# Optimization experiments

Measured on AMD Instinct MI355X. Metric: run time of the kernel, lower is better.

The kernel has to match this reference:

```python
import jax, jax.numpy as jnp
import numpy as np
from jax import lax

LRELU_SLOPE = 0.01  # torch nn.LeakyReLU default
BN_EPS = 1e-5


def _conv3(x, w, b):
    # LatticePad(3x3 stencil, center (1,1)) + LatticeConvolution on 'cp' lattice == SAME 3x3 conv
    y = lax.conv_general_dilated(x, w, (1, 1), 'SAME', dimension_numbers=('NCHW', 'OIHW', 'NCHW'))
    return y + b[None, :, None, None]


def _lrelu(x):
    return jnp.where(x >= 0, x, LRELU_SLOPE * x)


def _down2(x):
    # LatticeDownsample with D=[[2,0],[0,2]] on cp lattice: keep even coords
    return x[:, :, ::2, ::2]


def _up2(x):
    # LatticeUpsample with D=[[2,0],[0,2]]: zero insertion
    n, c, h, w = x.shape
    return jnp.zeros((n, c, 2 * h, 2 * w), x.dtype).at[:, :, ::2, ::2].set(x)


def setup_inputs() -> dict:
    key = jax.random.key(0)
    ks = iter(jax.random.split(key, 32))

    def w3(ci, co):
        return jax.random.normal(next(ks), (co, ci, 3, 3), jnp.float32) * (1.0 / np.sqrt(ci * 9.0))

    chans = [3, 64, 128, 256, 512, 1024]
    inp = {"x": jax.random.normal(next(ks), (2, 3, 512, 512), jnp.float32)}
    for i in range(5):
        inp[f"w_d{i}"] = w3(chans[i], chans[i + 1])
        inp[f"b_d{i}"] = jnp.zeros((chans[i + 1],), jnp.float32)
    inp["w_in"] = w3(1024, 1024)
    inp["b_in"] = jnp.zeros((1024,), jnp.float32)
    inp["gamma"] = jnp.ones((1024,), jnp.float32)
    inp["beta"] = jnp.zeros((1024,), jnp.float32)
    up_io = [(1024, 512), (512, 256), (256, 128), (128, 64), (64, 64)]
    for i, (ci, co) in enumerate(up_io):
        inp[f"w_u{i}"] = w3(ci, co)
        inp[f"b_u{i}"] = jnp.zeros((co,), jnp.float32)
    inp["w_ep"] = jax.random.normal(next(ks), (3, 64), jnp.float32) * 0.125
    inp["b_ep"] = jnp.zeros((3,), jnp.float32)
    return inp


def reference(x, w_d0, b_d0, w_d1, b_d1, w_d2, b_d2, w_d3, b_d3, w_d4, b_d4,
              w_in, b_in, gamma, beta,
              w_u0, b_u0, w_u1, b_u1, w_u2, b_u2, w_u3, b_u3, w_u4, b_u4,
              w_ep, b_ep):
    h = x
    # encoder: conv3x3 + LeakyReLU, then stride-2 subsample (skip outputs unused: skip=False in config)
    for w, b in [(w_d0, b_d0), (w_d1, b_d1), (w_d2, b_d2), (w_d3, b_d3), (w_d4, b_d4)]:
        h = _down2(_lrelu(_conv3(h, w, b)))
    # innermost ConvBlock: conv + BatchNorm (batch stats, training mode) + LeakyReLU
    h = _conv3(h, w_in, b_in)
    mu = h.mean((0, 2, 3), keepdims=True)
    var = h.var((0, 2, 3), keepdims=True)
    h = (h - mu) / jnp.sqrt(var + BN_EPS) * gamma[None, :, None, None] + beta[None, :, None, None]
    h = _lrelu(h)
    # decoder: zero-insert upsample, conv3x3 + LeakyReLU
    for w, b in [(w_u0, b_u0), (w_u1, b_u1), (w_u2, b_u2), (w_u3, b_u3), (w_u4, b_u4)]:
        h = _lrelu(_conv3(_up2(h), w, b))
    # epilogue 1x1 conv
    return jnp.einsum('nchw,oc->nohw', h, w_ep) + b_ep[None, :, None, None]
```

## Files before the change

kernel.cpp:

```cpp
#include <hip/hip_runtime.h>
#include <math.h>

#define LRELU_SLOPE 0.01f
#define BN_EPS 1e-5f

__device__ __forceinline__ float lrelu_f(float v) { return v >= 0.f ? v : LRELU_SLOPE * v; }

template <int MODE, int CC, bool PARTIAL>
__global__ __launch_bounds__(256, 2) void conv3_kernel(
    const float* __restrict__ in, const float* __restrict__ wgt,
    const float* __restrict__ bias, float* __restrict__ out,
    int Cin, int Hin, int Win, int Cout, int Ho, int Wo, int apply_act,
    int segCi, int cogY, size_t seg_stride)
{
  constexpr int IH = (MODE == 1) ? 17 : 10;
  constexpr int IW = (MODE == 1) ? 33 : 18;
  constexpr int IP = (MODE == 1) ? 36 : 20;
  __shared__ __align__(16) float s_in[CC * IH * IP];
  __shared__ __align__(16) float s_w[CC * 9 * 64];

  const int tid = threadIdx.x;
  const int tx  = tid & 15;
  const int ty  = tid >> 4;
  const int row = ty >> 1;
  const int xh  = (ty & 1) * 8;

  const int tilesX = Wo >> 4;
  const int x0   = (blockIdx.x % tilesX) * 16;
  const int y0   = (blockIdx.x / tilesX) * 8;
  const int cog0 = (blockIdx.y % cogY) * 64;
  const int seg  = blockIdx.y / cogY;
  const int ci_begin = seg * segCi;
  const int n    = blockIdx.z;
  if (PARTIAL) out += (size_t)seg * seg_stride;

  const size_t HWin = (size_t)Hin * Win;
  const float* inN = in + (size_t)n * Cin * HWin;

  float acc[4][8];
#pragma unroll
  for (int a = 0; a < 4; a++)
#pragma unroll
    for (int b = 0; b < 8; b++) acc[a][b] = 0.f;

  for (int ci0 = 0; ci0 < segCi; ci0 += CC) {
    const int chunk = (segCi - ci0 < CC) ? (segCi - ci0) : CC;
    __syncthreads();
    const int tot = chunk * (IH * IW);
    for (int idx = tid; idx < tot; idx += 256) {
      const int ci  = idx / (IH * IW);
      const int rem = idx - ci * (IH * IW);
      const int r   = rem / IW;
      const int c   = rem - r * IW;
      float v = 0.f;
      const int gci = ci_begin + ci0 + ci;
      if (MODE == 1) {
        const int gy = 2 * y0 - 1 + r;
        const int gx = 2 * x0 - 1 + c;
        if (gy >= 0 && gy < Hin && gx >= 0 && gx < Win)
          v = inN[(size_t)gci * HWin + (size_t)gy * Win + gx];
        const int dst = (c & 1) ? (20 + (c >> 1)) : (c >> 1);
        s_in[(ci * IH + r) * IP + dst] = v;
      } else {
        const int gy = y0 - 1 + r;
        const int gx = x0 - 1 + c;
        if (gy >= 0 && gy < Hin && gx >= 0 && gx < Win)
          v = inN[(size_t)gci * HWin + (size_t)gy * Win + gx];
        s_in[(ci * IH + r) * IP + c] = v;
      }
    }
    const int e9 = chunk * 9;
    const int wtot = e9 * 64;
    for (int idx = tid; idx < wtot; idx += 256) {
      const int co = idx & 63;
      const int e  = idx >> 6;
      s_w[e * 64 + co] = wgt[(size_t)(cog0 + co) * Cin * 9 + (size_t)(ci_begin + ci0) * 9 + e];
    }
    __syncthreads();

    auto body = [&](int ci) {
#pragma unroll
      for (int ky = 0; ky < 3; ky++) {
        if (MODE == 1) {
          const int base = (ci * IH + 2 * row + ky) * IP;
          const float4 ea = *(const float4*)&s_in[base + xh];
          const float4 eb = *(const float4*)&s_in[base + xh + 4];
          const float  e8 = s_in[base + xh + 8];
          const float4 oa = *(const float4*)&s_in[base + 20 + xh];
          const float4 ob = *(const float4*)&s_in[base + 24 + xh];
          const float ev[9] = {ea.x, ea.y, ea.z, ea.w, eb.x, eb.y, eb.z, eb.w, e8};
          const float ov[8] = {oa.x, oa.y, oa.z, oa.w, ob.x, ob.y, ob.z, ob.w};
#pragma unroll
          for (int kx = 0; kx < 3; kx++) {
            const int e = ci * 9 + ky * 3 + kx;
            const float4 w4 = *(const float4*)&s_w[e * 64 + (tx << 2)];
            const float wv[4] = {w4.x, w4.y, w4.z, w4.w};
#pragma unroll
            for (int j = 0; j < 8; j++) {
              const float xv = (kx == 0) ? ev[j] : ((kx == 1) ? ov[j] : ev[j + 1]);
#pragma unroll
              for (int k = 0; k < 4; k++) acc[k][j] += wv[k] * xv;
            }
          }
        } else {
          const int base = (ci * IH + row + ky) * IP + xh;
          const float4 a4 = *(const float4*)&s_in[base];
          const float4 b4 = *(const float4*)&s_in[base + 4];
          const float2 c2 = *(const float2*)&s_in[base + 8];
          const float iv[10] = {a4.x, a4.y, a4.z, a4.w, b4.x, b4.y, b4.z, b4.w, c2.x, c2.y};
#pragma unroll
          for (int kx = 0; kx < 3; kx++) {
            const int e = ci * 9 + ky * 3 + kx;
            const float4 w4 = *(const float4*)&s_w[e * 64 + (tx << 2)];
            const float wv[4] = {w4.x, w4.y, w4.z, w4.w};
#pragma unroll
            for (int j = 0; j < 8; j++) {
              const float xv = iv[j + kx];
#pragma unroll
              for (int k = 0; k < 4; k++) acc[k][j] += wv[k] * xv;
            }
          }
        }
      }
    };
    if (chunk == CC) {
#pragma unroll
      for (int ci = 0; ci < CC; ci++) body(ci);
    } else {
      for (int ci = 0; ci < chunk; ci++) body(ci);
    }
  }

#pragma unroll
  for (int k = 0; k < 4; k++) {
    const int co = cog0 + tx * 4 + k;
    float* op = out + ((size_t)((size_t)n * Cout + co) * Ho + (y0 + row)) * Wo + x0 + xh;
    float4 v0, v1;
    if constexpr (PARTIAL) {
      v0.x = acc[k][0]; v0.y = acc[k][1]; v0.z = acc[k][2]; v0.w = acc[k][3];
      v1.x = acc[k][4]; v1.y = acc[k][5]; v1.z = acc[k][6]; v1.w = acc[k][7];
    } else {
      const float b = bias[co];
      v0.x = acc[k][0] + b; v0.y = acc[k][1] + b; v0.z = acc[k][2] + b; v0.w = acc[k][3] + b;
      v1.x = acc[k][4] + b; v1.y = acc[k][5] + b; v1.z = acc[k][6] + b; v1.w = acc[k][7] + b;
      if (apply_act) {
        v0.x = lrelu_f(v0.x); v0.y = lrelu_f(v0.y); v0.z = lrelu_f(v0.z); v0.w = lrelu_f(v0.w);
        v1.x = lrelu_f(v1.x); v1.y = lrelu_f(v1.y); v1.z = lrelu_f(v1.z); v1.w = lrelu_f(v1.w);
      }
    }
    *reinterpret_cast<float4*>(op) = v0;
    *reinterpret_cast<float4*>(op + 4) = v1;
  }
}

template <int NQ, int KCO, int CC, bool EPI, bool PARTIAL>
__global__ __launch_bounds__(256, 2) void up_conv_kernel(
    const float* __restrict__ in, const float* __restrict__ wgt,
    const float* __restrict__ bias, float* __restrict__ out,
    int Cin, int Hin, int Win, int Cout, int Ho, int Wo,
    int segCi, int cogY, size_t seg_stride,
    const float* __restrict__ w_ep, const float* __restrict__ b_ep)
{
  constexpr int NCO = 16 * KCO;
  constexpr int LOG = (KCO == 4) ? 6 : 5;
  constexpr int TQ = 2 * NQ;
  constexpr int T  = 4 * TQ;
  constexpr int IR = 4 * NQ + 1;
  constexpr int PR = IR + 1;
  __shared__ __align__(16) float s_in[CC * IR * PR];
  __shared__ __align__(16) float s_w[CC * 9 * NCO];
  __shared__ float s_epi[EPI ? 3 * 16 * 17 : 1];

  const int tid = threadIdx.x;
  const int tx  = tid & 15;
  const int ty  = tid >> 4;
  const int Qy  = ty >> 2;
  const int Qx  = ty & 3;

  const int tilesX = Wo / T;
  const int x0   = (blockIdx.x % tilesX) * T;
  const int y0   = (blockIdx.x / tilesX) * T;
  const int cog0 = (blockIdx.y % cogY) * NCO;
  const int seg  = blockIdx.y / cogY;
  const int ci_begin = seg * segCi;
  const int n    = blockIdx.z;
  if (PARTIAL) out += (size_t)seg * seg_stride;
  const int r0 = y0 >> 1;
  const int c0 = x0 >> 1;

  const size_t HWin = (size_t)Hin * Win;
  const float* inN = in + (size_t)n * Cin * HWin;

  float acc[KCO][TQ][TQ];
#pragma unroll
  for (int k = 0; k < KCO; k++)
#pragma unroll
    for (int i = 0; i < TQ; i++)
#pragma unroll
      for (int j = 0; j < TQ; j++) acc[k][i][j] = 0.f;

  for (int ci0 = 0; ci0 < segCi; ci0 += CC) {
    __syncthreads();
    const int tot = CC * (IR * IR);
    for (int idx = tid; idx < tot; idx += 256) {
      const int ci  = idx / (IR * IR);
      const int rem = idx - ci * (IR * IR);
      const int r   = rem / IR;
      const int c   = rem - r * IR;
      const int gy = r0 + r, gx = c0 + c;
      float v = 0.f;
      if (gy < Hin && gx < Win)
        v = inN[(size_t)(ci_begin + ci0 + ci) * HWin + (size_t)gy * Win + gx];
      s_in[(ci * IR + r) * PR + c] = v;
    }
    const int wtot = CC * 9 * NCO;
    for (int idx = tid; idx < wtot; idx += 256) {
      const int co = idx & (NCO - 1);
      const int e  = idx >> LOG;
      s_w[e * NCO + co] = wgt[(size_t)(cog0 + co) * Cin * 9 + (size_t)(ci_begin + ci0) * 9 + e];
    }
    __syncthreads();

#pragma unroll
    for (int ci = 0; ci < CC; ci++) {
      float iv[NQ + 1][NQ + 1];
#pragma unroll
      for (int dr = 0; dr <= NQ; dr++)
#pragma unroll
        for (int dc = 0; dc <= NQ; dc++)
          iv[dr][dc] = s_in[(ci * IR + NQ * Qy + dr) * PR + NQ * Qx + dc];
#pragma unroll
      for (int t = 0; t < 9; t++) {
        const int ky = t / 3, kx = t % 3;
        float wv[KCO];
        if constexpr (KCO == 4) {
          const float4 w4 = *(const float4*)&s_w[(ci * 9 + t) * 64 + (tx << 2)];
          wv[0] = w4.x; wv[1] = w4.y; wv[2] = w4.z; wv[3] = w4.w;
        } else {
          const float2 w2 = *(const float2*)&s_w[(ci * 9 + t) * 32 + (tx << 1)];
          wv[0] = w2.x; wv[1] = w2.y;
        }
        const int pr  = (ky == 1) ? 0 : 1;
        const int drr = (ky == 2) ? 1 : 0;
        const int pc  = (kx == 1) ? 0 : 1;
        const int dcc = (kx == 2) ? 1 : 0;
#pragma unroll
        for (int a = 0; a < NQ; a++)
#pragma unroll
          for (int b = 0; b < NQ; b++) {
            const float xv = iv[a + drr][b + dcc];
#pragma unroll
            for (int k = 0; k < KCO; k++)
              acc[k][2 * a + pr][2 * b + pc] += wv[k] * xv;
          }
      }
    }
  }

  if (!EPI) {
#pragma unroll
    for (int k = 0; k < KCO; k++) {
      const int co = cog0 + tx * KCO + k;
      const float bv = PARTIAL ? 0.f : bias[co];
#pragma unroll
      for (int i = 0; i < TQ; i++) {
        const int y = y0 + TQ * Qy + i;
        float* op = out + ((size_t)((size_t)n * Cout + co) * Ho + y) * Wo + x0 + TQ * Qx;
        if constexpr (NQ == 2) {
          float4 v;
          if constexpr (PARTIAL) {
            v.x = acc[k][i][0]; v.y = acc[k][i][1]; v.z = acc[k][i][2]; v.w = acc[k][i][3];
          } else {
            v.x = lrelu_f(acc[k][i][0] + bv); v.y = lrelu_f(acc[k][i][1] + bv);
            v.z = lrelu_f(acc[k][i][2] + bv); v.w = lrelu_f(acc[k][i][3] + bv);
          }
          *reinterpret_cast<float4*>(op) = v;
        } else {
          float2 v;
          if constexpr (PARTIAL) {
            v.x = acc[k][i][0]; v.y = acc[k][i][1];
          } else {
            v.x = lrelu_f(acc[k][i][0] + bv); v.y = lrelu_f(acc[k][i][1] + bv);
          }
          *reinterpret_cast<float2*>(op) = v;
        }
      }
    }
  } else {
    float wep[3][KCO];
#pragma unroll
    for (int o = 0; o < 3; o++)
#pragma unroll
      for (int k = 0; k < KCO; k++) wep[o][k] = w_ep[o * 64 + tx * KCO + k];
    const float bv[KCO] = {bias[tx * KCO + 0], bias[tx * KCO + 1],
                           bias[tx * KCO + 2], bias[tx * KCO + 3]};
    __syncthreads();
#pragma unroll
    for (int i = 0; i < TQ; i++)
#pragma unroll
      for (int j = 0; j < TQ; j++) {
        float h[KCO];
#pragma unroll
        for (int k = 0; k < KCO; k++) h[k] = lrelu_f(acc[k][i][j] + bv[k]);
        float s0 = 0.f, s1 = 0.f, s2 = 0.f;
#pragma unroll
        for (int k = 0; k < KCO; k++) {
          s0 += wep[0][k] * h[k]; s1 += wep[1][k] * h[k]; s2 += wep[2][k] * h[k];
        }
#pragma unroll
        for (int m = 1; m < 16; m <<= 1) {
          s0 += __shfl_xor(s0, m); s1 += __shfl_xor(s1, m); s2 += __shfl_xor(s2, m);
        }
        if (tx < 3) {
          const float sv = (tx == 0) ? s0 : ((tx == 1) ? s1 : s2);
          s_epi[tx * 272 + (TQ * Qy + i) * 17 + TQ * Qx + j] = sv;
        }
      }
    __syncthreads();
    if (tid < 192) {
      const int o   = tid >> 6;
      const int rem = tid & 63;
      const int row = rem >> 2;
      const int xq  = (rem & 3) << 2;
      const float be = b_ep[o];
      float4 v;
      v.x = s_epi[o * 272 + row * 17 + xq + 0] + be;
      v.y = s_epi[o * 272 + row * 17 + xq + 1] + be;
      v.z = s_epi[o * 272 + row * 17 + xq + 2] + be;
      v.w = s_epi[o * 272 + row * 17 + xq + 3] + be;
      float* op = out + ((size_t)((size_t)n * 3 + o) * Ho + (y0 + row)) * Wo + x0 + xq;
      *reinterpret_cast<float4*>(op) = v;
    }
  }
}

__global__ __launch_bounds__(256) void reduce_bias_act_kernel(
    float* __restrict__ dst, const float* __restrict__ part,
    const float* __restrict__ bias, int total4, int HW, int Cout,
    int S, int seg_stride4, int act)
{
  const int i = blockIdx.x * 256 + threadIdx.x;
  if (i >= total4) return;
  const float4* p = (const float4*)part;
  float4 s = p[i];
  for (int k = 1; k < S; k++) {
    const float4 v = p[i + (size_t)k * seg_stride4];
    s.x += v.x; s.y += v.y; s.z += v.z; s.w += v.w;
  }
  const int co = ((i << 2) / HW) % Cout;
  const float b = bias[co];
  s.x += b; s.y += b; s.z += b; s.w += b;
  if (act) { s.x = lrelu_f(s.x); s.y = lrelu_f(s.y); s.z = lrelu_f(s.z); s.w = lrelu_f(s.w); }
  ((float4*)dst)[i] = s;
}

__global__ __launch_bounds__(256) void bn_lrelu_kernel(
    float* __restrict__ h, const float* __restrict__ gamma, const float* __restrict__ beta)
{
  const int c = blockIdx.x;
  const int t = threadIdx.x;
  const size_t i0 = (size_t)c * 256 + t;
  const size_t i1 = (size_t)(1024 + c) * 256 + t;
  const float v0 = h[i0], v1 = h[i1];
  float s = v0 + v1;
  float q = v0 * v0 + v1 * v1;
  for (int o = 32; o > 0; o >>= 1) { s += __shfl_down(s, o); q += __shfl_down(q, o); }
  __shared__ float sh[8];
  __shared__ float param[2];
  const int wid = t >> 6, lane = t & 63;
  if (lane == 0) { sh[wid] = s; sh[4 + wid] = q; }
  __syncthreads();
  if (t == 0) {
    const float S = sh[0] + sh[1] + sh[2] + sh[3];
    const float Q = sh[4] + sh[5] + sh[6] + sh[7];
    const float mean = S * (1.f / 512.f);
    const float var = Q * (1.f / 512.f) - mean * mean;
    const float scale = gamma[c] / sqrtf(var + BN_EPS);
    param[0] = scale;
    param[1] = beta[c] - mean * scale;
  }
  __syncthreads();
  const float sc = param[0], sf = param[1];
  h[i0] = lrelu_f(v0 * sc + sf);
  h[i1] = lrelu_f(v1 * sc + sf);
}

extern "C" void kernel_launch(void* const* d_in, const int* in_sizes, int n_in,
                              void* d_out, int out_size, void* d_ws, size_t ws_size,
                              hipStream_t stream)
{
  (void)in_sizes; (void)n_in; (void)out_size; (void)ws_size;
  const float* x     = (const float*)d_in[0];
  const float* w_d0  = (const float*)d_in[1];
  const float* b_d0  = (const float*)d_in[2];
  const float* w_d1  = (const float*)d_in[3];
  const float* b_d1  = (const float*)d_in[4];
  const float* w_d2  = (const float*)d_in[5];
  const float* b_d2  = (const float*)d_in[6];
  const float* w_d3  = (const float*)d_in[7];
  const float* b_d3  = (const float*)d_in[8];
  const float* w_d4  = (const float*)d_in[9];
  const float* b_d4  = (const float*)d_in[10];
  const float* w_in  = (const float*)d_in[11];
  const float* b_in  = (const float*)d_in[12];
  const float* gamma = (const float*)d_in[13];
  const float* beta  = (const float*)d_in[14];
  const float* w_u0  = (const float*)d_in[15];
  const float* b_u0  = (const float*)d_in[16];
  const float* w_u1  = (const float*)d_in[17];
  const float* b_u1  = (const float*)d_in[18];
  const float* w_u2  = (const float*)d_in[19];
  const float* b_u2  = (const float*)d_in[20];
  const float* w_u3  = (const float*)d_in[21];
  const float* b_u3  = (const float*)d_in[22];
  const float* w_u4  = (const float*)d_in[23];
  const float* b_u4  = (const float*)d_in[24];
  const float* w_ep  = (const float*)d_in[25];
  const float* b_ep  = (const float*)d_in[26];

  float* W = (float*)d_ws;
  float* e0   = W;
  float* e1   = W + 8388608;
  float* Pd2  = W;
  float* e2   = W + 12582912;
  float* Pd3  = W + 4194304;
  float* e3   = W;
  float* Pd4  = W + 4194304;
  float* e4   = W + 1048576;
  float* Pin  = W + 4194304;
  float* Fb   = W + 1572864;
  float* G    = W;
  float* Pu0  = W + 2097152;
  float* H    = W + 10485760;
  float* Pu1  = W + 1048576;
  float* I    = W + 12582912;
  float* Pu2  = W;
  float* J    = W;
  float* outp = (float*)d_out;

  const dim3 blk(256);
  conv3_kernel<1, 8, false><<<dim3(512,   1, 2), blk, 0, stream>>>(x,  w_d0, b_d0, e0,    3, 512, 512,   64, 256, 256, 1,   3,  1, 0);
  conv3_kernel<1, 8, false><<<dim3(128,   2, 2), blk, 0, stream>>>(e0, w_d1, b_d1, e1,   64, 256, 256,  128, 128, 128, 1,  64,  2, 0);
  conv3_kernel<1, 8, true ><<<dim3( 32,   8, 2), blk, 0, stream>>>(e1, w_d2, b_d2, Pd2, 128, 128, 128,  256,  64,  64, 1,  64,  4, 2097152);
  reduce_bias_act_kernel<<<dim3(2048), blk, 0, stream>>>(e2, Pd2, b_d2, 524288, 4096, 256, 2, 524288, 1);
  conv3_kernel<1, 8, true ><<<dim3(  8,  32, 2), blk, 0, stream>>>(e2, w_d3, b_d3, Pd3, 256,  64,  64,  512,  32,  32, 1,  64,  8, 1048576);
  reduce_bias_act_kernel<<<dim3(1024), blk, 0, stream>>>(e3, Pd3, b_d3, 262144, 1024, 512, 4, 262144, 1);
  conv3_kernel<1, 8, true ><<<dim3(  2, 128, 2), blk, 0, stream>>>(e3, w_d4, b_d4, Pd4, 512,  32,  32, 1024,  16,  16, 1,  64, 16, 524288);
  reduce_bias_act_kernel<<<dim3( 512), blk, 0, stream>>>(e4, Pd4, b_d4, 131072, 256, 1024, 8, 131072, 1);
  conv3_kernel<0, 8, true ><<<dim3(  2, 128, 2), blk, 0, stream>>>(e4, w_in, b_in, Pin, 1024, 16,  16, 1024,  16,  16, 0, 128, 16, 524288);
  reduce_bias_act_kernel<<<dim3( 512), blk, 0, stream>>>(Fb, Pin, b_in, 131072, 256, 1024, 8, 131072, 0);
  bn_lrelu_kernel<<<dim3(1024), blk, 0, stream>>>(Fb, gamma, beta);
  up_conv_kernel<2, 4, 8, false, true ><<<dim3(  4, 64, 2), blk, 0, stream>>>(Fb, w_u0, b_u0, Pu0, 1024, 16,  16,  512,  32,  32, 128, 8, 1048576, nullptr, nullptr);
  reduce_bias_act_kernel<<<dim3(1024), blk, 0, stream>>>(G, Pu0, b_u0, 262144, 1024, 512, 8, 262144, 1);
  up_conv_kernel<2, 4, 8, false, true ><<<dim3( 16, 16, 2), blk, 0, stream>>>(G,  w_u1, b_u1, Pu1,  512, 32,  32,  256,  64,  64, 128, 4, 2097152, nullptr, nullptr);
  reduce_bias_act_kernel<<<dim3(2048), blk, 0, stream>>>(H, Pu1, b_u1, 524288, 4096, 256, 4, 524288, 1);
  up_conv_kernel<2, 4, 8, false, true ><<<dim3( 64,  4, 2), blk, 0, stream>>>(H,  w_u2, b_u2, Pu2,  256, 64,  64,  128, 128, 128, 128, 2, 4194304, nullptr, nullptr);
  reduce_bias_act_kernel<<<dim3(4096), blk, 0, stream>>>(I, Pu2, b_u2, 1048576, 16384, 128, 2, 1048576, 1);
  up_conv_kernel<2, 4, 8, false, false><<<dim3(256,  1, 2), blk, 0, stream>>>(I,  w_u3, b_u3, J,    128, 128, 128,   64, 256, 256, 128, 1, 0, nullptr, nullptr);
  up_conv_kernel<2, 4, 8, true,  false><<<dim3(1024, 1, 2), blk, 0, stream>>>(J,  w_u4, b_u4, outp,  64, 256, 256,   64, 512, 512,  64, 1, 0, w_ep, b_ep);
}
```

Measured before the change: 1.741 ms.

## Enlarge per-thread output tiles in encoder and decoder convolutions for register reuse

The encoder conv kernel now computes two output rows per thread over a 16-row tile, loading the nine weight vectors once per input channel and reusing input rows across both outputs. A new up_wide_kernel gives each thread a 4x8 output patch over a 32x16 tile for the three largest decoder layers, with the fused 1x1 epilogue moved into it. Split-K segmentation and workspace offsets are rearranged to match. The aim is fewer shared-memory loads per FMA and less redundant halo staging. The cost is more accumulator registers (up to 128 floats), which under launch_bounds(256,2) may cause spills or lower occupancy, and fewer blocks per layer.

After: 2.152 ms. 23.6% more time.

```diff
diff --git a/kernel.cpp b/kernel.cpp
--- a/kernel.cpp
+++ b/kernel.cpp
@@ -13,7 +13,7 @@
     int Cin, int Hin, int Win, int Cout, int Ho, int Wo, int apply_act,
     int segCi, int cogY, size_t seg_stride)
 {
-  constexpr int IH = (MODE == 1) ? 17 : 10;
+  constexpr int IH = (MODE == 1) ? 33 : 18;
   constexpr int IW = (MODE == 1) ? 33 : 18;
   constexpr int IP = (MODE == 1) ? 36 : 20;
   __shared__ __align__(16) float s_in[CC * IH * IP];
@@ -22,12 +22,12 @@
   const int tid = threadIdx.x;
   const int tx  = tid & 15;
   const int ty  = tid >> 4;
-  const int row = ty >> 1;
   const int xh  = (ty & 1) * 8;
+  const int rp  = ty >> 1;
 
   const int tilesX = Wo >> 4;
   const int x0   = (blockIdx.x % tilesX) * 16;
-  const int y0   = (blockIdx.x / tilesX) * 8;
+  const int y0   = (blockIdx.x / tilesX) * 16;
   const int cog0 = (blockIdx.y % cogY) * 64;
   const int seg  = blockIdx.y / cogY;
   const int ci_begin = seg * segCi;
@@ -37,11 +37,13 @@
   const size_t HWin = (size_t)Hin * Win;
   const float* inN = in + (size_t)n * Cin * HWin;
 
-  float acc[4][8];
+  float acc[4][2][8];
 #pragma unroll
   for (int a = 0; a < 4; a++)
 #pragma unroll
-    for (int b = 0; b < 8; b++) acc[a][b] = 0.f;
+    for (int r = 0; r < 2; r++)
+#pragma unroll
+      for (int b = 0; b < 8; b++) acc[a][r][b] = 0.f;
 
   for (int ci0 = 0; ci0 < segCi; ci0 += CC) {
     const int chunk = (segCi - ci0 < CC) ? (segCi - ci0) : CC;
@@ -79,10 +81,14 @@
     __syncthreads();
 
     auto body = [&](int ci) {
-#pragma unroll
-      for (int ky = 0; ky < 3; ky++) {
-        if (MODE == 1) {
-          const int base = (ci * IH + 2 * row + ky) * IP;
+      float4 wq[9];
+#pragma unroll
+      for (int t = 0; t < 9; t++)
+        wq[t] = *(const float4*)&s_w[(ci * 9 + t) * 64 + (tx << 2)];
+      if (MODE == 1) {
+#pragma unroll
+        for (int ir = 0; ir < 5; ir++) {
+          const int base = (ci * IH + 4 * rp + ir) * IP;
           const float4 ea = *(const float4*)&s_in[base + xh];
           const float4 eb = *(const float4*)&s_in[base + xh + 4];
           const float  e8 = s_in[base + xh + 8];
@@ -91,33 +97,44 @@
           const float ev[9] = {ea.x, ea.y, ea.z, ea.w, eb.x, eb.y, eb.z, eb.w, e8};
           const float ov[8] = {oa.x, oa.y, oa.z, oa.w, ob.x, ob.y, ob.z, ob.w};
 #pragma unroll
-          for (int kx = 0; kx < 3; kx++) {
-            const int e = ci * 9 + ky * 3 + kx;
-            const float4 w4 = *(const float4*)&s_w[e * 64 + (tx << 2)];
-            const float wv[4] = {w4.x, w4.y, w4.z, w4.w};
-#pragma unroll
-            for (int j = 0; j < 8; j++) {
-              const float xv = (kx == 0) ? ev[j] : ((kx == 1) ? ov[j] : ev[j + 1]);
-#pragma unroll
-              for (int k = 0; k < 4; k++) acc[k][j] += wv[k] * xv;
+          for (int r = 0; r < 2; r++) {
+            const int ky = ir - 2 * r;
+            if (ky < 0 || ky > 2) continue;
+#pragma unroll
+            for (int kx = 0; kx < 3; kx++) {
+              const float4 w4 = wq[ky * 3 + kx];
+              const float wv[4] = {w4.x, w4.y, w4.z, w4.w};
+#pragma unroll
+              for (int j = 0; j < 8; j++) {
+                const float xv = (kx == 0) ? ev[j] : ((kx == 1) ? ov[j] : ev[j + 1]);
+#pragma unroll
+                for (int k = 0; k < 4; k++) acc[k][r][j] += wv[k] * xv;
+              }
             }
           }
-        } else {
-          const int base = (ci * IH + row + ky) * IP + xh;
+        }
+      } else {
+#pragma unroll
+        for (int ir = 0; ir < 4; ir++) {
+          const int base = (ci * IH + 2 * rp + ir) * IP + xh;
           const float4 a4 = *(const float4*)&s_in[base];
           const float4 b4 = *(const float4*)&s_in[base + 4];
           const float2 c2 = *(const float2*)&s_in[base + 8];
           const float iv[10] = {a4.x, a4.y, a4.z, a4.w, b4.x, b4.y, b4.z, b4.w, c2.x, c2.y};
 #pragma unroll
-          for (int kx = 0; kx < 3; kx++) {
-            const int e = ci * 9 + ky * 3 + kx;
-            const float4 w4 = *(const float4*)&s_w[e * 64 + (tx << 2)];
-            const float wv[4] = {w4.x, w4.y, w4.z, w4.w};
-#pragma unroll
-            for (int j = 0; j < 8; j++) {
-              const float xv = iv[j + kx];
-#pragma unroll
-              for (int k = 0; k < 4; k++) acc[k][j] += wv[k] * xv;
+          for (int r = 0; r < 2; r++) {
+            const int ky = ir - r;
+            if (ky < 0 || ky > 2) continue;
+#pragma unroll
+            for (int kx = 0; kx < 3; kx++) {
+              const float4 w4 = wq[ky * 3 + kx];
+              const float wv[4] = {w4.x, w4.y, w4.z, w4.w};
+#pragma unroll
+              for (int j = 0; j < 8; j++) {
+                const float xv = iv[j + kx];
+#pragma unroll
+                for (int k = 0; k < 4; k++) acc[k][r][j] += wv[k] * xv;
+              }
             }
           }
         }
@@ -134,22 +151,184 @@
 #pragma unroll
   for (int k = 0; k < 4; k++) {
     const int co = cog0 + tx * 4 + k;
-    float* op = out + ((size_t)((size_t)n * Cout + co) * Ho + (y0 + row)) * Wo + x0 + xh;
-    float4 v0, v1;
-    if constexpr (PARTIAL) {
-      v0.x = acc[k][0]; v0.y = acc[k][1]; v0.z = acc[k][2]; v0.w = acc[k][3];
-      v1.x = acc[k][4]; v1.y = acc[k][5]; v1.z = acc[k][6]; v1.w = acc[k][7];
-    } else {
-      const float b = bias[co];
-      v0.x = acc[k][0] + b; v0.y = acc[k][1] + b; v0.z = acc[k][2] + b; v0.w = acc[k][3] + b;
-      v1.x = acc[k][4] + b; v1.y = acc[k][5] + b; v1.z = acc[k][6] + b; v1.w = acc[k][7] + b;
-      if (apply_act) {
+    const float b = PARTIAL ? 0.f : bias[co];
+#pragma unroll
+    for (int r = 0; r < 2; r++) {
+      float* op = out + ((size_t)((size_t)n * Cout + co) * Ho + (y0 + 2 * rp + r)) * Wo + x0 + xh;
+      float4 v0, v1;
+      v0.x = acc[k][r][0] + b; v0.y = acc[k][r][1] + b; v0.z = acc[k][r][2] + b; v0.w = acc[k][r][3] + b;
+      v1.x = acc[k][r][4] + b; v1.y = acc[k][r][5] + b; v1.z = acc[k][r][6] + b; v1.w = acc[k][r][7] + b;
+      if (!PARTIAL && apply_act) {
         v0.x = lrelu_f(v0.x); v0.y = lrelu_f(v0.y); v0.z = lrelu_f(v0.z); v0.w = lrelu_f(v0.w);
         v1.x = lrelu_f(v1.x); v1.y = lrelu_f(v1.y); v1.z = lrelu_f(v1.z); v1.w = lrelu_f(v1.w);
       }
-    }
-    *reinterpret_cast<float4*>(op) = v0;
-    *reinterpret_cast<float4*>(op + 4) = v1;
+      *reinterpret_cast<float4*>(op) = v0;
+      *reinterpret_cast<float4*>(op + 4) = v1;
+    }
+  }
+}
+
+template <int CC, bool EPI, bool PARTIAL>
+__global__ __launch_bounds__(256, 2) void up_wide_kernel(
+    const float* __restrict__ in, const float* __restrict__ wgt,
+    const float* __restrict__ bias, float* __restrict__ out,
+    int Cin, int Hin, int Win, int Cout, int Ho, int Wo,
+    int segCi, int cogY, size_t seg_stride,
+    const float* __restrict__ w_ep, const float* __restrict__ b_ep)
+{
+  constexpr int IR = 9;
+  constexpr int ICW = 17;
+  constexpr int PC = 20;
+  __shared__ __align__(16) float s_in[CC * IR * PC];
+  __shared__ __align__(16) float s_w[CC * 9 * 64];
+  __shared__ float s_epi[EPI ? 3 * 16 * 33 : 1];
+
+  const int tid = threadIdx.x;
+  const int tx  = tid & 15;
+  const int ty  = tid >> 4;
+  const int qx0 = (ty & 3) * 4;
+  const int qy0 = (ty >> 2) * 2;
+
+  const int tilesX = Wo >> 5;
+  const int x0   = (blockIdx.x % tilesX) * 32;
+  const int y0   = (blockIdx.x / tilesX) * 16;
+  const int cog0 = (blockIdx.y % cogY) * 64;
+  const int seg  = blockIdx.y / cogY;
+  const int ci_begin = seg * segCi;
+  const int n    = blockIdx.z;
+  if (PARTIAL) out += (size_t)seg * seg_stride;
+  const int r0 = y0 >> 1;
+  const int c0 = x0 >> 1;
+
+  const size_t HWin = (size_t)Hin * Win;
+  const float* inN = in + (size_t)n * Cin * HWin;
+
+  float acc[4][4][8];
+#pragma unroll
+  for (int k = 0; k < 4; k++)
+#pragma unroll
+    for (int i = 0; i < 4; i++)
+#pragma unroll
+      for (int j = 0; j < 8; j++) acc[k][i][j] = 0.f;
+
+  for (int ci0 = 0; ci0 < segCi; ci0 += CC) {
+    __syncthreads();
+    const int tot = CC * (IR * ICW);
+    for (int idx = tid; idx < tot; idx += 256) {
+      const int ci  = idx / (IR * ICW);
+      const int rem = idx - ci * (IR * ICW);
+      const int r   = rem / ICW;
+      const int c   = rem - r * ICW;
+      const int gy = r0 + r, gx = c0 + c;
+      float v = 0.f;
+      if (gy < Hin && gx < Win)
+        v = inN[(size_t)(ci_begin + ci0 + ci) * HWin + (size_t)gy * Win + gx];
+      s_in[(ci * IR + r) * PC + c] = v;
+    }
+    const int wtot = CC * 9 * 64;
+    for (int idx = tid; idx < wtot; idx += 256) {
+      const int co = idx & 63;
+      const int e  = idx >> 6;
+      s_w[e * 64 + co] = wgt[(size_t)(cog0 + co) * Cin * 9 + (size_t)(ci_begin + ci0) * 9 + e];
+    }
+    __syncthreads();
+
+#pragma unroll
+    for (int ci = 0; ci < CC; ci++) {
+      float iv[3][5];
+#pragma unroll
+      for (int dr = 0; dr < 3; dr++) {
+        const int base = (ci * IR + qy0 + dr) * PC + qx0;
+        const float4 a4 = *(const float4*)&s_in[base];
+        iv[dr][0] = a4.x; iv[dr][1] = a4.y; iv[dr][2] = a4.z; iv[dr][3] = a4.w;
+        iv[dr][4] = s_in[base + 4];
+      }
+#pragma unroll
+      for (int t = 0; t < 9; t++) {
+        const int ky = t / 3, kx = t % 3;
+        const float4 w4 = *(const float4*)&s_w[(ci * 9 + t) * 64 + (tx << 2)];
+        const float wv[4] = {w4.x, w4.y, w4.z, w4.w};
+        const int pr  = (ky == 1) ? 0 : 1;
+        const int drr = (ky == 2) ? 1 : 0;
+        const int pc  = (kx == 1) ? 0 : 1;
+        const int dcc = (kx == 2) ? 1 : 0;
+#pragma unroll
+        for (int a = 0; a < 2; a++)
+#pragma unroll
+          for (int b = 0; b < 4; b++) {
+            const float xv = iv[a + drr][b + dcc];
+#pragma unroll
+            for (int k = 0; k < 4; k++)
+              acc[k][2 * a + pr][2 * b + pc] += wv[k] * xv;
+          }
+      }
+    }
+  }
+
+  if (!EPI) {
+#pragma unroll
+    for (int k = 0; k < 4; k++) {
+      const int co = cog0 + tx * 4 + k;
+      const float bv = PARTIAL ? 0.f : bias[co];
+#pragma unroll
+      for (int i = 0; i < 4; i++) {
+        const int y = y0 + 2 * qy0 + i;
+        float* op = out + ((size_t)((size_t)n * Cout + co) * Ho + y) * Wo + x0 + 2 * qx0;
+        float4 v0, v1;
+        v0.x = acc[k][i][0] + bv; v0.y = acc[k][i][1] + bv; v0.z = acc[k][i][2] + bv; v0.w = acc[k][i][3] + bv;
+        v1.x = acc[k][i][4] + bv; v1.y = acc[k][i][5] + bv; v1.z = acc[k][i][6] + bv; v1.w = acc[k][i][7] + bv;
+        if (!PARTIAL) {
+          v0.x = lrelu_f(v0.x); v0.y = lrelu_f(v0.y); v0.z = lrelu_f(v0.z); v0.w = lrelu_f(v0.w);
+          v1.x = lrelu_f(v1.x); v1.y = lrelu_f(v1.y); v1.z = lrelu_f(v1.z); v1.w = lrelu_f(v1.w);
+        }
+        *reinterpret_cast<float4*>(op) = v0;
+        *reinterpret_cast<float4*>(op + 4) = v1;
+      }
+    }
+  } else {
+    float wep[3][4];
+#pragma unroll
+    for (int o = 0; o < 3; o++)
+#pragma unroll
+      for (int k = 0; k < 4; k++) wep[o][k] = w_ep[o * 64 + tx * 4 + k];
+    const float bv[4] = {bias[tx * 4 + 0], bias[tx * 4 + 1], bias[tx * 4 + 2], bias[tx * 4 + 3]};
+    __syncthreads();
+#pragma unroll
+    for (int i = 0; i < 4; i++)
+#pragma unroll
+      for (int j = 0; j < 8; j++) {
+        float h[4];
+#pragma unroll
+        for (int k = 0; k < 4; k++) h[k] = lrelu_f(acc[k][i][j] + bv[k]);
+        float s0 = 0.f, s1 = 0.f, s2 = 0.f;
+#pragma unroll
+        for (int k = 0; k < 4; k++) {
+          s0 += wep[0][k] * h[k]; s1 += wep[1][k] * h[k]; s2 += wep[2][k] * h[k];
+        }
+#pragma unroll
+        for (int m = 1; m < 16; m <<= 1) {
+          s0 += __shfl_xor(s0, m); s1 += __shfl_xor(s1, m); s2 += __shfl_xor(s2, m);
+        }
+        if (tx < 3) {
+          const float sv = (tx == 0) ? s0 : ((tx == 1) ? s1 : s2);
+          s_epi[tx * 528 + (2 * qy0 + i) * 33 + 2 * qx0 + j] = sv;
+        }
+      }
+    __syncthreads();
+    for (int idx = tid; idx < 384; idx += 256) {
+      const int o   = idx >> 7;
+      const int rem = idx & 127;
+      const int row = rem >> 3;
+      const int c4  = (rem & 7) << 2;
+      const float be = b_ep[o];
+      float4 v;
+      v.x = s_epi[o * 528 + row * 33 + c4 + 0] + be;
+      v.y = s_epi[o * 528 + row * 33 + c4 + 1] + be;
+      v.z = s_epi[o * 528 + row * 33 + c4 + 2] + be;
+      v.w = s_epi[o * 528 + row * 33 + c4 + 3] + be;
+      float* op = out + ((size_t)((size_t)n * 3 + o) * Ho + (y0 + row)) * Wo + x0 + c4;
+      *reinterpret_cast<float4*>(op) = v;
+    }
   }
 }
 
@@ -169,7 +348,6 @@
   constexpr int PR = IR + 1;
   __shared__ __align__(16) float s_in[CC * IR * PR];
   __shared__ __align__(16) float s_w[CC * 9 * NCO];
-  __shared__ float s_epi[EPI ? 3 * 16 * 17 : 1];
 
   const int tid = threadIdx.x;
   const int tx  = tid & 15;
@@ -233,13 +411,8 @@
       for (int t = 0; t < 9; t++) {
         const int ky = t / 3, kx = t % 3;
         float wv[KCO];
-        if constexpr (KCO == 4) {
-          const float4 w4 = *(const float4*)&s_w[(ci * 9 + t) * 64 + (tx << 2)];
-          wv[0] = w4.x; wv[1] = w4.y; wv[2] = w4.z; wv[3] = w4.w;
-        } else {
-          const float2 w2 = *(const float2*)&s_w[(ci * 9 + t) * 32 + (tx << 1)];
-          wv[0] = w2.x; wv[1] = w2.y;
-        }
+        const float4 w4 = *(const float4*)&s_w[(ci * 9 + t) * 64 + (tx << 2)];
+        wv[0] = w4.x; wv[1] = w4.y; wv[2] = w4.z; wv[3] = w4.w;
         const int pr  = (ky == 1) ? 0 : 1;
         const int drr = (ky == 2) ? 1 : 0;
         const int pc  = (kx == 1) ? 0 : 1;
@@ -257,78 +430,21 @@
     }
   }
 
-  if (!EPI) {
-#pragma unroll
-    for (int k = 0; k < KCO; k++) {
-      const int co = cog0 + tx * KCO + k;
-      const float bv = PARTIAL ? 0.f : bias[co];
-#pragma unroll
-      for (int i = 0; i < TQ; i++) {
-        const int y = y0 + TQ * Qy + i;
-        float* op = out + ((size_t)((size_t)n * Cout + co) * Ho + y) * Wo + x0 + TQ * Qx;
-        if constexpr (NQ == 2) {
-          float4 v;
-          if constexpr (PARTIAL) {
-            v.x = acc[k][i][0]; v.y = acc[k][i][1]; v.z = acc[k][i][2]; v.w = acc[k][i][3];
-          } else {
-            v.x = lrelu_f(acc[k][i][0] + bv); v.y = lrelu_f(acc[k][i][1] + bv);
-            v.z = lrelu_f(acc[k][i][2] + bv); v.w = lrelu_f(acc[k][i][3] + bv);
-          }
-          *reinterpret_cast<float4*>(op) = v;
-        } else {
-          float2 v;
-          if constexpr (PARTIAL) {
-            v.x = acc[k][i][0]; v.y = acc[k][i][1];
-          } else {
-            v.x = lrelu_f(acc[k][i][0] + bv); v.y = lrelu_f(acc[k][i][1] + bv);
-          }
-          *reinterpret_cast<float2*>(op) = v;
-        }
-      }
-    }
-  } else {
-    float wep[3][KCO];
-#pragma unroll
-    for (int o = 0; o < 3; o++)
-#pragma unroll
-      for (int k = 0; k < KCO; k++) wep[o][k] = w_ep[o * 64 + tx * KCO + k];
-    const float bv[KCO] = {bias[tx * KCO + 0], bias[tx * KCO + 1],
-                           bias[tx * KCO + 2], bias[tx * KCO + 3]};
-    __syncthreads();
-#pragma unroll
-    for (int i = 0; i < TQ; i++)
-#pragma unroll
-      for (int j = 0; j < TQ; j++) {
-        float h[KCO];
-#pragma unroll
-        for (int k = 0; k < KCO; k++) h[k] = lrelu_f(acc[k][i][j] + bv[k]);
-        float s0 = 0.f, s1 = 0.f, s2 = 0.f;
-#pragma unroll
-        for (int k = 0; k < KCO; k++) {
-          s0 += wep[0][k] * h[k]; s1 += wep[1][k] * h[k]; s2 += wep[2][k] * h[k];
-        }
-#pragma unroll
-        for (int m = 1; m < 16; m <<= 1) {
-          s0 += __shfl_xor(s0, m); s1 += __shfl_xor(s1, m); s2 += __shfl_xor(s2, m);
-        }
-        if (tx < 3) {
-          const float sv = (tx == 0) ? s0 : ((tx == 1) ? s1 : s2);
-          s_epi[tx * 272 + (TQ * Qy + i) * 17 + TQ * Qx + j] = sv;
-        }
-      }
-    __syncthreads();
-    if (tid < 192) {
-      const int o   = tid >> 6;
-      const int rem = tid & 63;
-      const int row = rem >> 2;
-      const int xq  = (rem & 3) << 2;
-      const float be = b_ep[o];
+#pragma unroll
+  for (int k = 0; k < KCO; k++) {
+    const int co = cog0 + tx * KCO + k;
+    const float bv = PARTIAL ? 0.f : bias[co];
+#pragma unroll
+    for (int i = 0; i < TQ; i++) {
+      const int y = y0 + TQ * Qy + i;
+      float* op = out + ((size_t)((size_t)n * Cout + co) * Ho + y) * Wo + x0 + TQ * Qx;
       float4 v;
-      v.x = s_epi[o * 272 + row * 17 + xq + 0] + be;
-      v.y = s_epi[o * 272 + row * 17 + xq + 1] + be;
-      v.z = s_epi[o * 272 + row * 17 + xq + 2] + be;
-      v.w = s_epi[o * 272 + row * 17 + xq + 3] + be;
-      float* op = out + ((size_t)((size_t)n * 3 + o) * Ho + (y0 + row)) * Wo + x0 + xq;
+      if constexpr (PARTIAL) {
+        v.x = acc[k][i][0]; v.y = acc[k][i][1]; v.z = acc[k][i][2]; v.w = acc[k][i][3];
+      } else {
+        v.x = lrelu_f(acc[k][i][0] + bv); v.y = lrelu_f(acc[k][i][1] + bv);
+        v.z = lrelu_f(acc[k][i][2] + bv); v.w = lrelu_f(acc[k][i][3] + bv);
+      }
       *reinterpret_cast<float4*>(op) = v;
     }
   }
@@ -419,43 +535,43 @@
   const float* b_ep  = (const float*)d_in[26];
 
   float* W = (float*)d_ws;
-  float* e0   = W;
-  float* e1   = W + 8388608;
-  float* Pd2  = W;
-  float* e2   = W + 12582912;
-  float* Pd3  = W + 4194304;
-  float* e3   = W;
-  float* Pd4  = W + 4194304;
-  float* e4   = W + 1048576;
-  float* Pin  = W + 4194304;
-  float* Fb   = W + 1572864;
-  float* G    = W;
-  float* Pu0  = W + 2097152;
-  float* H    = W + 10485760;
-  float* Pu1  = W + 1048576;
-  float* I    = W + 12582912;
-  float* Pu2  = W;
-  float* J    = W;
+  float* e0  = W;
+  float* e1  = W + 8388608;
+  float* Pd2 = W;
+  float* e2  = W + 12582912;
+  float* Pd3 = W;
+  float* e3  = W + 14680064;
+  float* Pd4 = W;
+  float* e4  = W + 15204352;
+  float* Pin = W;
+  float* Fb  = W + 15728640;
+  float* Pu0 = W;
+  float* G   = W + 8388608;
+  float* Pu1 = W;
+  float* H   = W + 9437184;
+  float* Pu2 = W;
+  float* I   = W + 11534336;
+  float* J   = W;
   float* outp = (float*)d_out;
 
   const dim3 blk(256);
-  conv3_kernel<1, 8, false><<<dim3(512,   1, 2), blk, 0, stream>>>(x,  w_d0, b_d0, e0,    3, 512, 512,   64, 256, 256, 1,   3,  1, 0);
-  conv3_kernel<1, 8, false><<<dim3(128,   2, 2), blk, 0, stream>>>(e0, w_d1, b_d1, e1,   64, 256, 256,  128, 128, 128, 1,  64,  2, 0);
-  conv3_kernel<1, 8, true ><<<dim3( 32,   8, 2), blk, 0, stream>>>(e1, w_d2, b_d2, Pd2, 128, 128, 128,  256,  64,  64, 1,  64,  4, 2097152);
-  reduce_bias_act_kernel<<<dim3(2048), blk, 0, stream>>>(e2, Pd2, b_d2, 524288, 4096, 256, 2, 524288, 1);
-  conv3_kernel<1, 8, true ><<<dim3(  8,  32, 2), blk, 0, stream>>>(e2, w_d3, b_d3, Pd3, 256,  64,  64,  512,  32,  32, 1,  64,  8, 1048576);
-  reduce_bias_act_kernel<<<dim3(1024), blk, 0, stream>>>(e3, Pd3, b_d3, 262144, 1024, 512, 4, 262144, 1);
-  conv3_kernel<1, 8, true ><<<dim3(  2, 128, 2), blk, 0, stream>>>(e3, w_d4, b_d4, Pd4, 512,  32,  32, 1024,  16,  16, 1,  64, 16, 524288);
-  reduce_bias_act_kernel<<<dim3( 512), blk, 0, stream>>>(e4, Pd4, b_d4, 131072, 256, 1024, 8, 131072, 1);
-  conv3_kernel<0, 8, true ><<<dim3(  2, 128, 2), blk, 0, stream>>>(e4, w_in, b_in, Pin, 1024, 16,  16, 1024,  16,  16, 0, 128, 16, 524288);
-  reduce_bias_act_kernel<<<dim3( 512), blk, 0, stream>>>(Fb, Pin, b_in, 131072, 256, 1024, 8, 131072, 0);
+  conv3_kernel<1, 4, false><<<dim3(256,   1, 2), blk, 0, stream>>>(x,  w_d0, b_d0, e0,    3, 512, 512,   64, 256, 256, 1,   3,  1, 0);
+  conv3_kernel<1, 8, false><<<dim3( 64,   2, 2), blk, 0, stream>>>(e0, w_d1, b_d1, e1,   64, 256, 256,  128, 128, 128, 1,  64,  2, 0);
+  conv3_kernel<1, 8, true ><<<dim3( 16,  16, 2), blk, 0, stream>>>(e1, w_d2, b_d2, Pd2, 128, 128, 128,  256,  64,  64, 1,  32,  4, 2097152);
+  reduce_bias_act_kernel<<<dim3(2048), blk, 0, stream>>>(e2, Pd2, b_d2, 524288, 4096, 256, 4, 524288, 1);
+  conv3_kernel<1, 8, true ><<<dim3(  4,  64, 2), blk, 0, stream>>>(e2, w_d3, b_d3, Pd3, 256,  64,  64,  512,  32,  32, 1,  32,  8, 1048576);
+  reduce_bias_act_kernel<<<dim3(1024), blk, 0, stream>>>(e3, Pd3, b_d3, 262144, 1024, 512, 8, 262144, 1);
+  conv3_kernel<1, 8, true ><<<dim3(  1, 256, 2), blk, 0, stream>>>(e3, w_d4, b_d4, Pd4, 512,  32,  32, 1024,  16,  16, 1,  32, 16, 524288);
+  reduce_bias_act_kernel<<<dim3( 512), blk, 0, stream>>>(e4, Pd4, b_d4, 131072, 256, 1024, 16, 131072, 1);
+  conv3_kernel<0, 8, true ><<<dim3(  1, 256, 2), blk, 0, stream>>>(e4, w_in, b_in, Pin, 1024, 16,  16, 1024,  16,  16, 0,  64, 16, 524288);
+  reduce_bias_act_kernel<<<dim3( 512), blk, 0, stream>>>(Fb, Pin, b_in, 131072, 256, 1024, 16, 131072, 0);
   bn_lrelu_kernel<<<dim3(1024), blk, 0, stream>>>(Fb, gamma, beta);
   up_conv_kernel<2, 4, 8, false, true ><<<dim3(  4, 64, 2), blk, 0, stream>>>(Fb, w_u0, b_u0, Pu0, 1024, 16,  16,  512,  32,  32, 128, 8, 1048576, nullptr, nullptr);
   reduce_bias_act_kernel<<<dim3(1024), blk, 0, stream>>>(G, Pu0, b_u0, 262144, 1024, 512, 8, 262144, 1);
   up_conv_kernel<2, 4, 8, false, true ><<<dim3( 16, 16, 2), blk, 0, stream>>>(G,  w_u1, b_u1, Pu1,  512, 32,  32,  256,  64,  64, 128, 4, 2097152, nullptr, nullptr);
   reduce_bias_act_kernel<<<dim3(2048), blk, 0, stream>>>(H, Pu1, b_u1, 524288, 4096, 256, 4, 524288, 1);
-  up_conv_kernel<2, 4, 8, false, true ><<<dim3( 64,  4, 2), blk, 0, stream>>>(H,  w_u2, b_u2, Pu2,  256, 64,  64,  128, 128, 128, 128, 2, 4194304, nullptr, nullptr);
+  up_wide_kernel<8, false, true ><<<dim3( 32,  4, 2), blk, 0, stream>>>(H,  w_u2, b_u2, Pu2,  256, 64,  64,  128, 128, 128, 128, 2, 4194304, nullptr, nullptr);
   reduce_bias_act_kernel<<<dim3(4096), blk, 0, stream>>>(I, Pu2, b_u2, 1048576, 16384, 128, 2, 1048576, 1);
-  up_conv_kernel<2, 4, 8, false, false><<<dim3(256,  1, 2), blk, 0, stream>>>(I,  w_u3, b_u3, J,    128, 128, 128,   64, 256, 256, 128, 1, 0, nullptr, nullptr);
-  up_conv_kernel<2, 4, 8, true,  false><<<dim3(1024, 1, 2), blk, 0, stream>>>(J,  w_u4, b_u4, outp,  64, 256, 256,   64, 512, 512,  64, 1, 0, w_ep, b_ep);
+  up_wide_kernel<8, false, false><<<dim3(128,  1, 2), blk, 0, stream>>>(I,  w_u3, b_u3, J,    128, 128, 128,   64, 256, 256, 128, 1, 0, nullptr, nullptr);
+  up_wide_kernel<8, true,  false><<<dim3(512,  1, 2), blk, 0, stream>>>(J,  w_u4, b_u4, outp,  64, 256, 256,   64, 512, 512,  64, 1, 0, w_ep, b_ep);
 }
```
